# Optimization experiments

Hardware: AMD Instinct MI355X
Metric: run time of the kernel (lower is better)

## Reference

```python
import jax, jax.numpy as jnp
import numpy as np

N, S, K, D, H = 65536, 5, 4, 12, 48  # batch, sq_len, max_node_num, nodefeat_n1, lstm hidden


def setup_inputs() -> dict:
    key = jax.random.key(0)
    ks = jax.random.split(key, 32)
    f = lambda i, shape, s=0.1: jax.random.normal(ks[i], shape, dtype=jnp.float32) * s
    return {
        'nodes_feature': f(0, (N, S, K, 6), 1.0),
        'pos': f(1, (N, S, K, 6), 1.0),
        'attmat': jax.random.uniform(ks[2], (N, S, K, K), dtype=jnp.float32),
        'msg_w': f(3, (D, D)), 'msg_b': f(4, (D,)),
        'gru_w_ih': f(5, (3 * D, D)), 'gru_w_hh': f(6, (3 * D, D)),
        'gru_b_ih': f(7, (3 * D,)), 'gru_b_hh': f(8, (3 * D,)),
        'lstm_w_ih_fw': f(9, (4 * H, H)), 'lstm_w_hh_fw': f(10, (4 * H, H)),
        'lstm_b_ih_fw': f(11, (4 * H,)), 'lstm_b_hh_fw': f(12, (4 * H,)),
        'lstm_w_ih_bw': f(13, (4 * H, H)), 'lstm_w_hh_bw': f(14, (4 * H, H)),
        'lstm_b_ih_bw': f(15, (4 * H,)), 'lstm_b_hh_bw': f(16, (4 * H,)),
        'en1_w': f(17, (H, 2 * H)), 'en1_b': f(18, (H,)),
        'en2_w': f(19, (36, H)), 'en2_b': f(20, (36,)),
        'en3_w': f(21, (6, 36)), 'en3_b': f(22, (6,)),
    }


def _gru_cell(x, h, w_ih, w_hh, b_ih, b_hh):
    # torch.nn.GRU single step: gates ordered r, z, n
    gi = x @ w_ih.T + b_ih
    gh = h @ w_hh.T + b_hh
    ir, iz, inn = jnp.split(gi, 3, axis=-1)
    hr, hz, hn = jnp.split(gh, 3, axis=-1)
    r = jax.nn.sigmoid(ir + hr)
    z = jax.nn.sigmoid(iz + hz)
    n = jnp.tanh(inn + r * hn)
    return (1.0 - z) * n + z * h


def _lstm_dir(x, w_ih, w_hh, b_ih, b_hh):
    # x: [T, N, H]; torch.nn.LSTM gates ordered i, f, g, o. Returns final hidden [N, H].
    nb = x.shape[1]
    hh = w_hh.shape[1]
    def step(carry, xt):
        h, c = carry
        g = xt @ w_ih.T + b_ih + h @ w_hh.T + b_hh
        i, fg, gg, o = jnp.split(g, 4, axis=-1)
        c = jax.nn.sigmoid(fg) * c + jax.nn.sigmoid(i) * jnp.tanh(gg)
        h = jax.nn.sigmoid(o) * jnp.tanh(c)
        return (h, c), None
    init = (jnp.zeros((nb, hh), x.dtype), jnp.zeros((nb, hh), x.dtype))
    (h, _), _ = jax.lax.scan(step, init, x)
    return h


def reference(nodes_feature, pos, attmat, msg_w, msg_b,
              gru_w_ih, gru_w_hh, gru_b_ih, gru_b_hh,
              lstm_w_ih_fw, lstm_w_hh_fw, lstm_b_ih_fw, lstm_b_hh_fw,
              lstm_w_ih_bw, lstm_w_hh_bw, lstm_b_ih_bw, lstm_b_hh_bw,
              en1_w, en1_b, en2_w, en2_b, en3_w, en3_b):
    node_feat = jnp.concatenate([nodes_feature, pos], axis=-1)  # [N,S,K,12]

    def message_pass(h):
        # message_fun on all neighbor states, attention-weighted sum, GRU update.
        m_all = h @ msg_w.T + msg_b                       # [N,S,K,12]
        m_v = jnp.einsum('bsnw,bswd->bsnd', attmat, m_all)  # [N,S,K,12]
        return _gru_cell(m_v, h, gru_w_ih, gru_w_hh, gru_b_ih, gru_b_hh)

    h = message_pass(node_feat)  # pass 0 (reads node_feat for h_v and h_w)
    h = message_pass(h)          # pass 1 (reads pass-0 hidden state)

    # hidden_node_state is stored [..., feat, node]; view(5,-1) flattens (feat, node)
    x = jnp.transpose(h, (0, 1, 3, 2)).reshape(h.shape[0], S, D * K)  # [N,S,48]
    xt = jnp.transpose(x, (1, 0, 2))  # [S,N,48]
    h_fw = _lstm_dir(xt, lstm_w_ih_fw, lstm_w_hh_fw, lstm_b_ih_fw, lstm_b_hh_fw)
    h_bw = _lstm_dir(xt[::-1], lstm_w_ih_bw, lstm_w_hh_bw, lstm_b_ih_bw, lstm_b_hh_bw)
    hn = jnp.concatenate([h_fw, h_bw], axis=-1)  # [N,96] == h_n.view(-1) per batch

    e = jax.nn.relu(hn @ en1_w.T + en1_b)
    e = jax.nn.relu(e @ en2_w.T + en2_b)
    return e @ en3_w.T + en3_b  # pred_label [N,6]
```

## Files before the change

kernel.cpp:

```cpp
#include <hip/hip_runtime.h>
#include <cstddef>

#define NB 65536
#define SL 5

typedef _Float16 f16;
typedef f16 half8 __attribute__((ext_vector_type(8)));
typedef float f32x4 __attribute__((ext_vector_type(4)));

__device__ __forceinline__ float sigm(float x) {
  return __builtin_amdgcn_rcpf(1.0f + __expf(-x));
}
__device__ __forceinline__ float tanh_f(float x) {
  return __builtin_fmaf(2.0f, __builtin_amdgcn_rcpf(1.0f + __expf(-2.0f * x)), -1.0f);
}
__device__ __forceinline__ unsigned int pkh2(float a, float b) {
  return (unsigned int)__builtin_bit_cast(unsigned short, (_Float16)a)
       | ((unsigned int)__builtin_bit_cast(unsigned short, (_Float16)b) << 16);
}
__device__ __forceinline__ float loh(unsigned int u) {
  return (float)__builtin_bit_cast(_Float16, (unsigned short)(u & 0xffffu));
}
__device__ __forceinline__ float hih(unsigned int u) {
  return (float)__builtin_bit_cast(_Float16, (unsigned short)(u >> 16));
}

__global__ __launch_bounds__(256) void prep_kernel(
    const float* __restrict__ wi_fw, const float* __restrict__ wh_fw,
    const float* __restrict__ bi_fw, const float* __restrict__ bh_fw,
    const float* __restrict__ wi_bw, const float* __restrict__ wh_bw,
    const float* __restrict__ bi_bw, const float* __restrict__ bh_bw,
    const float* __restrict__ msg_w, const float* __restrict__ msg_b,
    const float* __restrict__ gw_ih, const float* __restrict__ gw_hh,
    const float* __restrict__ gb_ih, const float* __restrict__ gb_hh,
    unsigned short* __restrict__ wfrag, float* __restrict__ bsum,
    unsigned short* __restrict__ mfrag, float* __restrict__ mbias)
{
  const int t = blockIdx.x * 256 + threadIdx.x;
  if (t < 36864) {
    const int i = t & 7, lane = (t >> 3) & 63, fid = t >> 9;
    const int kc = fid % 3, mt = (fid / 3) % 3, ug = (fid / 9) & 3, dir = fid / 36;
    const int k = kc * 32 + (lane >> 4) * 8 + i;
    const int r16 = lane & 15;
    const int j = ug * 12 + mt * 4 + (r16 >> 2);
    const int g = r16 & 3;
    const float* wi = dir ? wi_bw : wi_fw;
    const float* wh = dir ? wh_bw : wh_fw;
    const float v = (k < 48) ? wi[(g * 48 + j) * 48 + k] : wh[(g * 48 + j) * 48 + (k - 48)];
    wfrag[t] = __builtin_bit_cast(unsigned short, (_Float16)v);
  } else if (t < 37248) {
    const int q = t - 36864;
    const int r16 = q & 15, mt = (q >> 4) % 3, ug = (q / 48) & 3, dir = q / 192;
    const int j = ug * 12 + mt * 4 + (r16 >> 2);
    const int g = r16 & 3;
    const int row = g * 48 + j;
    bsum[q] = dir ? (bi_bw[row] + bh_bw[row]) : (bi_fw[row] + bh_fw[row]);
  } else if (t < 39296) {
    const int q = t - 37248;
    const int i = q & 7, lane = (q >> 3) & 63, fid = q >> 9;
    const int k = ((lane >> 4) << 3) + i;
    const int r16 = lane & 15;
    float v = 0.0f;
    if (fid == 0) {
      if (r16 < 12 && k >= 12 && k < 24) v = msg_w[r16 * 12 + (k - 12)];
    } else {
      const int R = (fid - 1) * 16 + r16;
      const int kind = R / 12, j = R % 12;
      if (kind == 0)      v = (k < 12) ? gw_ih[j * 12 + k]          : ((k < 24) ? gw_hh[j * 12 + (k - 12)] : 0.0f);
      else if (kind == 1) v = (k < 12) ? gw_ih[(12 + j) * 12 + k]   : ((k < 24) ? gw_hh[(12 + j) * 12 + (k - 12)] : 0.0f);
      else if (kind == 2) v = (k < 12) ? gw_ih[(24 + j) * 12 + k]   : 0.0f;
      else                v = (k >= 12 && k < 24) ? gw_hh[(24 + j) * 12 + (k - 12)] : 0.0f;
    }
    mfrag[q] = __builtin_bit_cast(unsigned short, (_Float16)v);
  } else if (t < 39360) {
    const int q = t - 39296;
    if (q < 16) mbias[q] = (q < 12) ? msg_b[q] : 0.0f;
    else {
      const int R = q - 16, kind = R / 12, j = R % 12;
      float v;
      if (kind == 0)      v = gb_ih[j] + gb_hh[j];
      else if (kind == 1) v = gb_ih[12 + j] + gb_hh[12 + j];
      else if (kind == 2) v = gb_ih[24 + j];
      else                v = gb_hh[24 + j];
      mbias[q] = v;
    }
  }
}

__global__ __launch_bounds__(256) void msg_mfma_kernel(
    const float* __restrict__ nf, const float* __restrict__ pos,
    const float* __restrict__ att,
    const unsigned short* __restrict__ mfrag, const float* __restrict__ mbias,
    unsigned short* __restrict__ xth)
{
  __shared__ unsigned short B_lds[256][40];
  __shared__ unsigned short g_lds[256][50];
  unsigned short* xbuf = &g_lds[0][0];

  const int tid  = threadIdx.x;
  const int lane = tid & 63;
  const int w    = __builtin_amdgcn_readfirstlane(tid >> 6);
  const int c16  = lane & 15;
  const int grp  = lane >> 4;
  const int own  = tid;
  const int node = own & 3;
  const int sl   = (own >> 6) * 16 + ((own >> 4) & 3) * 4 + ((own >> 2) & 3);

  half8 A1 = *reinterpret_cast<const half8*>(mfrag + (size_t)lane * 8);
  half8 A2[3];
#pragma unroll
  for (int mt = 0; mt < 3; ++mt)
    A2[mt] = *reinterpret_cast<const half8*>(mfrag + (size_t)((1 + mt) * 64 + lane) * 8);
  const f32x4 bias1 = *reinterpret_cast<const f32x4*>(mbias + grp * 4);
  f32x4 bias2[3];
#pragma unroll
  for (int mt = 0; mt < 3; ++mt)
    bias2[mt] = *reinterpret_cast<const f32x4*>(mbias + 16 + mt * 16 + grp * 4);

  {
    unsigned int* bz = reinterpret_cast<unsigned int*>(&B_lds[0][0]);
#pragma unroll
    for (int q = 0; q < 6; ++q)  bz[tid * 20 + q] = 0u;
#pragma unroll
    for (int q = 12; q < 16; ++q) bz[tid * 20 + q] = 0u;
  }

  const int sid = blockIdx.x * 64 + sl;
  const int s   = sid >> 16;
  const int b   = sid & (NB - 1);
  float h[12];
  {
    const size_t ib = ((size_t)(b * SL + s) * 4 + node) * 6;
    const float2* n2 = (const float2*)(nf  + ib);
    const float2* p2 = (const float2*)(pos + ib);
#pragma unroll
    for (int q = 0; q < 3; q++) {
      float2 v = n2[q]; h[q*2]   = v.x; h[q*2+1]   = v.y;
      float2 u = p2[q]; h[6+q*2] = u.x; h[6+q*2+1] = u.y;
    }
  }
  float ta[4];
  {
    float4 v = *(const float4*)(att + ((size_t)(b * SL + s) * 4 + node) * 4);
    ta[0] = v.x; ta[1] = v.y; ta[2] = v.z; ta[3] = v.w;
  }
  {
    unsigned int* bp = (unsigned int*)&B_lds[own][0];
#pragma unroll
    for (int d = 0; d < 6; ++d) bp[6 + d] = pkh2(h[2*d], h[2*d+1]);
  }
  __syncthreads();

#pragma unroll 1
  for (int pass = 0; pass < 2; ++pass) {
#pragma unroll
    for (int nt = 0; nt < 4; ++nt) {
      const int col = w * 64 + nt * 16 + c16;
      half8 B = *reinterpret_cast<const half8*>(&B_lds[col][grp * 8]);
      f32x4 C = __builtin_amdgcn_mfma_f32_16x16x32_f16(A1, B, bias1, 0, 0, 0);
      if (grp < 3) {
        unsigned int* gp = (unsigned int*)&g_lds[col][0];
        gp[grp * 2]     = pkh2(C[0], C[1]);
        gp[grp * 2 + 1] = pkh2(C[2], C[3]);
      }
    }
    __syncthreads();

    {
      const int cb = own & ~3;
      float mv[12];
#pragma unroll
      for (int d = 0; d < 12; ++d) mv[d] = 0.0f;
#pragma unroll
      for (int ww = 0; ww < 4; ++ww) {
        const float a = ta[ww];
        const unsigned int* gp = (const unsigned int*)&g_lds[cb + ww][0];
#pragma unroll
        for (int dq = 0; dq < 6; ++dq) {
          const unsigned int u = gp[dq];
          mv[2*dq]   = __builtin_fmaf(a, loh(u), mv[2*dq]);
          mv[2*dq+1] = __builtin_fmaf(a, hih(u), mv[2*dq+1]);
        }
      }
      unsigned int* bp = (unsigned int*)&B_lds[own][0];
#pragma unroll
      for (int d = 0; d < 6; ++d) bp[d] = pkh2(mv[2*d], mv[2*d+1]);
    }
    __syncthreads();

#pragma unroll
    for (int nt = 0; nt < 4; ++nt) {
      const int col = w * 64 + nt * 16 + c16;
      half8 B = *reinterpret_cast<const half8*>(&B_lds[col][grp * 8]);
      f32x4 C0 = __builtin_amdgcn_mfma_f32_16x16x32_f16(A2[0], B, bias2[0], 0, 0, 0);
      f32x4 C1 = __builtin_amdgcn_mfma_f32_16x16x32_f16(A2[1], B, bias2[1], 0, 0, 0);
      f32x4 C2 = __builtin_amdgcn_mfma_f32_16x16x32_f16(A2[2], B, bias2[2], 0, 0, 0);
      unsigned int* gp = (unsigned int*)&g_lds[col][0];
      gp[grp * 2]      = pkh2(C0[0], C0[1]);
      gp[grp * 2 + 1]  = pkh2(C0[2], C0[3]);
      gp[8 + grp * 2]     = pkh2(C1[0], C1[1]);
      gp[8 + grp * 2 + 1] = pkh2(C1[2], C1[3]);
      gp[16 + grp * 2]     = pkh2(C2[0], C2[1]);
      gp[16 + grp * 2 + 1] = pkh2(C2[2], C2[3]);
    }
    __syncthreads();

    {
      unsigned int ur[6], uz[6], ui[6], uh[6];
      const unsigned int* gq = (const unsigned int*)&g_lds[own][0];
#pragma unroll
      for (int jq = 0; jq < 6; ++jq) {
        ur[jq] = gq[jq];
        uz[jq] = gq[6 + jq];
        ui[jq] = gq[12 + jq];
        uh[jq] = gq[18 + jq];
      }
      if (pass) __syncthreads();
#pragma unroll
      for (int jq = 0; jq < 6; ++jq) {
        {
          const float r = sigm(loh(ur[jq])), z = sigm(loh(uz[jq]));
          const float g = tanh_f(loh(ui[jq]) + r * loh(uh[jq]));
          h[2*jq] = (1.0f - z) * g + z * h[2*jq];
        }
        {
          const float r = sigm(hih(ur[jq])), z = sigm(hih(uz[jq]));
          const float g = tanh_f(hih(ui[jq]) + r * hih(uh[jq]));
          h[2*jq+1] = (1.0f - z) * g + z * h[2*jq+1];
        }
      }
      if (pass == 0) {
        unsigned int* bp = (unsigned int*)&B_lds[own][0];
#pragma unroll
        for (int d = 0; d < 6; ++d) bp[6 + d] = pkh2(h[2*d], h[2*d+1]);
      } else {
#pragma unroll
        for (int d = 0; d < 12; ++d)
          xbuf[sl * 50 + d * 4 + node] =
              __builtin_bit_cast(unsigned short, (_Float16)h[d]);
      }
    }
    __syncthreads();
  }

  const int b0   = (blockIdx.x * 64) & (NB - 1);
  const int sblk = blockIdx.x >> 10;
#pragma unroll
  for (int ff = 0; ff < 12; ++ff) {
    const int f = w * 12 + ff;
    xth[(size_t)(sblk * 48 + f) * NB + b0 + lane] = xbuf[lane * 50 + f];
  }
}

__global__ __launch_bounds__(512) void lstm_mfma_kernel(
    const unsigned short* __restrict__ xth,
    const unsigned short* __restrict__ wfrag,
    const float* __restrict__ bsum,
    const float* __restrict__ e1w, const float* __restrict__ e1b,
    const float* __restrict__ e2w, const float* __restrict__ e2b,
    const float* __restrict__ e3w, const float* __restrict__ e3b,
    float* __restrict__ out)
{
  __shared__ float4 pool4[2496];
  float* pool = (float*)pool4;
  unsigned short* act = (unsigned short*)pool;
  float* hf  = pool;
  float* e1o = pool + 6656;
  float* e2o = pool;

  const int tid  = threadIdx.x;
  const int lane = tid & 63;
  const int w    = __builtin_amdgcn_readfirstlane(tid >> 6);
  const int dir  = w & 1;
  const int ug   = w >> 1;
  const int b0   = blockIdx.x * 64;
  const int col  = lane & 15;
  const int grp  = lane >> 4;

  half8 A[3][3];
#pragma unroll
  for (int mt = 0; mt < 3; ++mt)
#pragma unroll
    for (int kc = 0; kc < 3; ++kc) {
      const int fid = ((dir * 4 + ug) * 3 + mt) * 3 + kc;
      A[mt][kc] = *reinterpret_cast<const half8*>(wfrag + (size_t)(fid * 64 + lane) * 8);
    }
  f32x4 bias[3];
#pragma unroll
  for (int mt = 0; mt < 3; ++mt)
    bias[mt] = *reinterpret_cast<const f32x4*>(bsum + ((dir * 4 + ug) * 3 + mt) * 16 + grp * 4);

#pragma unroll
  for (int ff = 0; ff < 6; ++ff) {
    const int f = w * 6 + ff;
    act[(0 * 64 + lane) * 104 + f] = xth[(size_t)(0 * 48 + f) * NB + b0 + lane];
    act[(1 * 64 + lane) * 104 + f] = xth[(size_t)(4 * 48 + f) * NB + b0 + lane];
  }
#pragma unroll
  for (int jj = 0; jj < 12; ++jj)
    act[(dir * 64 + lane) * 104 + 48 + ug * 12 + jj] = 0;
  __syncthreads();

  float c[3][4];
#pragma unroll
  for (int mt = 0; mt < 3; ++mt)
#pragma unroll
    for (int nt = 0; nt < 4; ++nt) c[mt][nt] = 0.0f;

#pragma unroll 1
  for (int st = 0; st < 5; ++st) {
    float hvf[3][4];
#pragma unroll
    for (int nt = 0; nt < 4; ++nt) {
      const int n = nt * 16 + col;
      const unsigned short* ar = &act[(dir * 64 + n) * 104];
      half8 B0 = *reinterpret_cast<const half8*>(ar + grp * 8);
      half8 B1 = *reinterpret_cast<const half8*>(ar + 32 + grp * 8);
      half8 B2 = *reinterpret_cast<const half8*>(ar + 64 + grp * 8);
      f32x4 C0 = bias[0], C1 = bias[1], C2 = bias[2];
      C0 = __builtin_amdgcn_mfma_f32_16x16x32_f16(A[0][0], B0, C0, 0, 0, 0);
      C0 = __builtin_amdgcn_mfma_f32_16x16x32_f16(A[0][1], B1, C0, 0, 0, 0);
      C0 = __builtin_amdgcn_mfma_f32_16x16x32_f16(A[0][2], B2, C0, 0, 0, 0);
      C1 = __builtin_amdgcn_mfma_f32_16x16x32_f16(A[1][0], B0, C1, 0, 0, 0);
      C1 = __builtin_amdgcn_mfma_f32_16x16x32_f16(A[1][1], B1, C1, 0, 0, 0);
      C1 = __builtin_amdgcn_mfma_f32_16x16x32_f16(A[1][2], B2, C1, 0, 0, 0);
      C2 = __builtin_amdgcn_mfma_f32_16x16x32_f16(A[2][0], B0, C2, 0, 0, 0);
      C2 = __builtin_amdgcn_mfma_f32_16x16x32_f16(A[2][1], B1, C2, 0, 0, 0);
      C2 = __builtin_amdgcn_mfma_f32_16x16x32_f16(A[2][2], B2, C2, 0, 0, 0);
#pragma unroll
      for (int mt = 0; mt < 3; ++mt) {
        const f32x4 C = (mt == 0) ? C0 : (mt == 1) ? C1 : C2;
        const float cc = sigm(C[1]) * c[mt][nt] + sigm(C[0]) * tanh_f(C[2]);
        c[mt][nt] = cc;
        hvf[mt][nt] = sigm(C[3]) * tanh_f(cc);
      }
    }
    __syncthreads();
    if (st < 4) {
#pragma unroll
      for (int mt = 0; mt < 3; ++mt)
#pragma unroll
        for (int nt = 0; nt < 4; ++nt)
          act[(dir * 64 + nt * 16 + col) * 104 + 48 + ug * 12 + mt * 4 + grp] =
              __builtin_bit_cast(unsigned short, (_Float16)hvf[mt][nt]);
      const int s0 = st + 1, s1 = 3 - st;
#pragma unroll
      for (int ff = 0; ff < 6; ++ff) {
        const int f = w * 6 + ff;
        act[(0 * 64 + lane) * 104 + f] = xth[(size_t)(s0 * 48 + f) * NB + b0 + lane];
        act[(1 * 64 + lane) * 104 + f] = xth[(size_t)(s1 * 48 + f) * NB + b0 + lane];
      }
    } else {
#pragma unroll
      for (int mt = 0; mt < 3; ++mt)
#pragma unroll
        for (int nt = 0; nt < 4; ++nt)
          hf[(nt * 16 + col) * 100 + dir * 48 + ug * 12 + mt * 4 + grp] = hvf[mt][nt];
    }
    __syncthreads();
  }

  {
    float acc[6];
#pragma unroll
    for (int r = 0; r < 6; ++r) acc[r] = e1b[w * 6 + r];
#pragma unroll
    for (int q = 0; q < 24; ++q) {
      const float4 v = *reinterpret_cast<const float4*>(&hf[lane * 100 + q * 4]);
#pragma unroll
      for (int r = 0; r < 6; ++r) {
        const int rr = w * 6 + r;
        acc[r] = __builtin_fmaf(e1w[rr * 96 + q * 4 + 0], v.x, acc[r]);
        acc[r] = __builtin_fmaf(e1w[rr * 96 + q * 4 + 1], v.y, acc[r]);
        acc[r] = __builtin_fmaf(e1w[rr * 96 + q * 4 + 2], v.z, acc[r]);
        acc[r] = __builtin_fmaf(e1w[rr * 96 + q * 4 + 3], v.w, acc[r]);
      }
    }
    __syncthreads();
#pragma unroll
    for (int r = 0; r < 6; ++r)
      e1o[lane * 52 + w * 6 + r] = acc[r] > 0.0f ? acc[r] : 0.0f;
  }
  __syncthreads();

  {
    const int e2base = (w < 4) ? w * 5 : 20 + (w - 4) * 4;
    const int e2cnt  = (w < 4) ? 5 : 4;
    float acc[5];
#pragma unroll
    for (int r = 0; r < 5; ++r) acc[r] = (r < e2cnt) ? e2b[e2base + r] : 0.0f;
#pragma unroll
    for (int q = 0; q < 12; ++q) {
      const float4 v = *reinterpret_cast<const float4*>(&e1o[lane * 52 + q * 4]);
#pragma unroll
      for (int r = 0; r < 5; ++r) {
        if (r < e2cnt) {
          const int rr = e2base + r;
          acc[r] = __builtin_fmaf(e2w[rr * 48 + q * 4 + 0], v.x, acc[r]);
          acc[r] = __builtin_fmaf(e2w[rr * 48 + q * 4 + 1], v.y, acc[r]);
          acc[r] = __builtin_fmaf(e2w[rr * 48 + q * 4 + 2], v.z, acc[r]);
          acc[r] = __builtin_fmaf(e2w[rr * 48 + q * 4 + 3], v.w, acc[r]);
        }
      }
    }
    __syncthreads();
#pragma unroll
    for (int r = 0; r < 5; ++r)
      if (r < e2cnt) e2o[lane * 44 + e2base + r] = acc[r] > 0.0f ? acc[r] : 0.0f;
  }
  __syncthreads();

  if (w < 6) {
    float a = e3b[w];
#pragma unroll
    for (int q = 0; q < 9; ++q) {
      const float4 v = *reinterpret_cast<const float4*>(&e2o[lane * 44 + q * 4]);
      a = __builtin_fmaf(e3w[w * 36 + q * 4 + 0], v.x, a);
      a = __builtin_fmaf(e3w[w * 36 + q * 4 + 1], v.y, a);
      a = __builtin_fmaf(e3w[w * 36 + q * 4 + 2], v.z, a);
      a = __builtin_fmaf(e3w[w * 36 + q * 4 + 3], v.w, a);
    }
    out[(size_t)(b0 + lane) * 6 + w] = a;
  }
}

extern "C" void kernel_launch(void* const* d_in, const int* in_sizes, int n_in,
                              void* d_out, int out_size, void* d_ws, size_t ws_size,
                              hipStream_t stream)
{
  const float* nf    = (const float*)d_in[0];
  const float* pos   = (const float*)d_in[1];
  const float* att   = (const float*)d_in[2];
  const float* msg_w = (const float*)d_in[3];
  const float* msg_b = (const float*)d_in[4];
  const float* gw_ih = (const float*)d_in[5];
  const float* gw_hh = (const float*)d_in[6];
  const float* gb_ih = (const float*)d_in[7];
  const float* gb_hh = (const float*)d_in[8];
  const float* wi_fw = (const float*)d_in[9];
  const float* wh_fw = (const float*)d_in[10];
  const float* bi_fw = (const float*)d_in[11];
  const float* bh_fw = (const float*)d_in[12];
  const float* wi_bw = (const float*)d_in[13];
  const float* wh_bw = (const float*)d_in[14];
  const float* bi_bw = (const float*)d_in[15];
  const float* bh_bw = (const float*)d_in[16];
  const float* e1w   = (const float*)d_in[17];
  const float* e1b   = (const float*)d_in[18];
  const float* e2w   = (const float*)d_in[19];
  const float* e2b   = (const float*)d_in[20];
  const float* e3w   = (const float*)d_in[21];
  const float* e3b   = (const float*)d_in[22];

  unsigned short* xth   = (unsigned short*)d_ws;
  unsigned short* wfrag = xth + (size_t)SL * 48 * NB;
  float*          bsum  = (float*)(wfrag + 36864);
  unsigned short* mfrag = (unsigned short*)(bsum + 384);
  float*          mbias = (float*)(mfrag + 2048);
  float*          outp  = (float*)d_out;

  prep_kernel<<<154, 256, 0, stream>>>(
      wi_fw, wh_fw, bi_fw, bh_fw, wi_bw, wh_bw, bi_bw, bh_bw,
      msg_w, msg_b, gw_ih, gw_hh, gb_ih, gb_hh,
      wfrag, bsum, mfrag, mbias);

  msg_mfma_kernel<<<(NB * SL) / 64, 256, 0, stream>>>(
      nf, pos, att, mfrag, mbias, xth);

  lstm_mfma_kernel<<<NB / 64, 512, 0, stream>>>(
      xth, wfrag, bsum, e1w, e1b, e2w, e2b, e3w, e3b, outp);
}
```

Baseline: 127.2 us.

## Prefetch next LSTM step inputs into registers and shrink LDS footprint

The next timestep's x inputs are now loaded from global memory into registers at the top of each LSTM step, so their latency overlaps the MFMA and gate math instead of sitting after the barrier. LDS stores of the inputs are packed as 32-bit pairs, and the encoder layer-1 output is kept as fp16 in a smaller shared buffer. The total LDS allocation drops, which may allow more resident blocks. The cost is more live registers across the step loop and fp16 rounding of the first encoder activations.

```diff
diff --git a/kernel.cpp b/kernel.cpp
--- a/kernel.cpp
+++ b/kernel.cpp
@@ -17,6 +17,9 @@
 __device__ __forceinline__ unsigned int pkh2(float a, float b) {
   return (unsigned int)__builtin_bit_cast(unsigned short, (_Float16)a)
        | ((unsigned int)__builtin_bit_cast(unsigned short, (_Float16)b) << 16);
+}
+__device__ __forceinline__ unsigned int pku2(unsigned short a, unsigned short b) {
+  return (unsigned int)a | ((unsigned int)b << 16);
 }
 __device__ __forceinline__ float loh(unsigned int u) {
   return (float)__builtin_bit_cast(_Float16, (unsigned short)(u & 0xffffu));
@@ -261,12 +264,11 @@
     const float* __restrict__ e3w, const float* __restrict__ e3b,
     float* __restrict__ out)
 {
-  __shared__ float4 pool4[2496];
-  float* pool = (float*)pool4;
-  unsigned short* act = (unsigned short*)pool;
-  float* hf  = pool;
-  float* e1o = pool + 6656;
-  float* e2o = pool;
+  __shared__ __align__(16) unsigned char poolc[33536];
+  unsigned short* act = (unsigned short*)poolc;
+  float*          hf  = (float*)poolc;
+  unsigned short* e1o = (unsigned short*)(poolc + 26624);
+  float*          e2o = (float*)poolc;
 
   const int tid  = threadIdx.x;
   const int lane = tid & 63;
@@ -290,15 +292,25 @@
   for (int mt = 0; mt < 3; ++mt)
     bias[mt] = *reinterpret_cast<const f32x4*>(bsum + ((dir * 4 + ug) * 3 + mt) * 16 + grp * 4);
 
-#pragma unroll
-  for (int ff = 0; ff < 6; ++ff) {
-    const int f = w * 6 + ff;
-    act[(0 * 64 + lane) * 104 + f] = xth[(size_t)(0 * 48 + f) * NB + b0 + lane];
-    act[(1 * 64 + lane) * 104 + f] = xth[(size_t)(4 * 48 + f) * NB + b0 + lane];
-  }
-#pragma unroll
-  for (int jj = 0; jj < 12; ++jj)
-    act[(dir * 64 + lane) * 104 + 48 + ug * 12 + jj] = 0;
+  {
+    unsigned short xa[6], xb[6];
+#pragma unroll
+    for (int ff = 0; ff < 6; ++ff) {
+      const int f = w * 6 + ff;
+      xa[ff] = xth[(size_t)(0 * 48 + f) * NB + b0 + lane];
+      xb[ff] = xth[(size_t)(4 * 48 + f) * NB + b0 + lane];
+    }
+    unsigned int* a0 = (unsigned int*)&act[(0 * 64 + lane) * 104 + w * 6];
+    unsigned int* a1 = (unsigned int*)&act[(1 * 64 + lane) * 104 + w * 6];
+#pragma unroll
+    for (int u = 0; u < 3; ++u) {
+      a0[u] = pku2(xa[2*u], xa[2*u+1]);
+      a1[u] = pku2(xb[2*u], xb[2*u+1]);
+    }
+  }
+#pragma unroll
+  for (int jj = 0; jj < 6; ++jj)
+    *(unsigned int*)&act[(dir * 64 + lane) * 104 + 48 + ug * 12 + jj * 2] = 0u;
   __syncthreads();
 
   float c[3][4];
@@ -309,6 +321,17 @@
 
 #pragma unroll 1
   for (int st = 0; st < 5; ++st) {
+    unsigned short nxa[6], nxb[6];
+    if (st < 4) {
+      const int s0 = st + 1, s1 = 3 - st;
+#pragma unroll
+      for (int ff = 0; ff < 6; ++ff) {
+        const int f = w * 6 + ff;
+        nxa[ff] = xth[(size_t)(s0 * 48 + f) * NB + b0 + lane];
+        nxb[ff] = xth[(size_t)(s1 * 48 + f) * NB + b0 + lane];
+      }
+    }
+
     float hvf[3][4];
 #pragma unroll
     for (int nt = 0; nt < 4; ++nt) {
@@ -343,12 +366,12 @@
         for (int nt = 0; nt < 4; ++nt)
           act[(dir * 64 + nt * 16 + col) * 104 + 48 + ug * 12 + mt * 4 + grp] =
               __builtin_bit_cast(unsigned short, (_Float16)hvf[mt][nt]);
-      const int s0 = st + 1, s1 = 3 - st;
-#pragma unroll
-      for (int ff = 0; ff < 6; ++ff) {
-        const int f = w * 6 + ff;
-        act[(0 * 64 + lane) * 104 + f] = xth[(size_t)(s0 * 48 + f) * NB + b0 + lane];
-        act[(1 * 64 + lane) * 104 + f] = xth[(size_t)(s1 * 48 + f) * NB + b0 + lane];
+      unsigned int* a0 = (unsigned int*)&act[(0 * 64 + lane) * 104 + w * 6];
+      unsigned int* a1 = (unsigned int*)&act[(1 * 64 + lane) * 104 + w * 6];
+#pragma unroll
+      for (int u = 0; u < 3; ++u) {
+        a0[u] = pku2(nxa[2*u], nxa[2*u+1]);
+        a1[u] = pku2(nxb[2*u], nxb[2*u+1]);
       }
     } else {
 #pragma unroll
@@ -377,9 +400,13 @@
       }
     }
     __syncthreads();
-#pragma unroll
-    for (int r = 0; r < 6; ++r)
-      e1o[lane * 52 + w * 6 + r] = acc[r] > 0.0f ? acc[r] : 0.0f;
+    unsigned int* ep = (unsigned int*)&e1o[lane * 54];
+#pragma unroll
+    for (int u = 0; u < 3; ++u) {
+      const float a0 = acc[2*u]   > 0.0f ? acc[2*u]   : 0.0f;
+      const float a1 = acc[2*u+1] > 0.0f ? acc[2*u+1] : 0.0f;
+      ep[w * 3 + u] = pkh2(a0, a1);
+    }
   }
   __syncthreads();
 
@@ -389,17 +416,17 @@
     float acc[5];
 #pragma unroll
     for (int r = 0; r < 5; ++r) acc[r] = (r < e2cnt) ? e2b[e2base + r] : 0.0f;
-#pragma unroll
-    for (int q = 0; q < 12; ++q) {
-      const float4 v = *reinterpret_cast<const float4*>(&e1o[lane * 52 + q * 4]);
+    const unsigned int* eq = (const unsigned int*)&e1o[lane * 54];
+#pragma unroll
+    for (int q = 0; q < 24; ++q) {
+      const unsigned int u = eq[q];
+      const float v0 = loh(u), v1 = hih(u);
 #pragma unroll
       for (int r = 0; r < 5; ++r) {
         if (r < e2cnt) {
           const int rr = e2base + r;
-          acc[r] = __builtin_fmaf(e2w[rr * 48 + q * 4 + 0], v.x, acc[r]);
-          acc[r] = __builtin_fmaf(e2w[rr * 48 + q * 4 + 1], v.y, acc[r]);
-          acc[r] = __builtin_fmaf(e2w[rr * 48 + q * 4 + 2], v.z, acc[r]);
-          acc[r] = __builtin_fmaf(e2w[rr * 48 + q * 4 + 3], v.w, acc[r]);
+          acc[r] = __builtin_fmaf(e2w[rr * 48 + 2*q],     v0, acc[r]);
+          acc[r] = __builtin_fmaf(e2w[rr * 48 + 2*q + 1], v1, acc[r]);
         }
       }
     }
```

Result: slower. 163.5 us (+28.6%).
